# Performance work log

Measured on AMD Instinct MI355X. Metric: run time of the kernel, lower is better.

Reference implementation:

```python
import jax, jax.numpy as jnp
import numpy as np

FORGET_BIAS = 1.0  # TF BasicLSTMCell default


def setup_inputs() -> dict:
    key = jax.random.key(0)
    k1, k2, k3, k4 = jax.random.split(key, 4)
    B, T, E, H, V = 64, 128, 256, 1024, 32000
    x = jax.random.normal(k1, (B, T, E), dtype=jnp.float32)
    # fused LSTM kernel [(E+H), 4H], gate order i, j, f, o
    kernel = jax.random.normal(k2, (E + H, 4 * H), dtype=jnp.float32) * 0.05
    bias = jnp.zeros((4 * H,), dtype=jnp.float32)
    w_out = jax.random.normal(k3, (H, V), dtype=jnp.float32) * 0.01
    b_out = jax.random.normal(k4, (V,), dtype=jnp.float32)
    return {"x": x, "kernel": kernel, "bias": bias, "w_out": w_out, "b_out": b_out}


def _lstm_last_hidden(x, kernel, bias):
    B, T, E = x.shape
    H = kernel.shape[1] // 4
    c0 = jnp.zeros((B, H), dtype=x.dtype)
    h0 = jnp.zeros((B, H), dtype=x.dtype)

    def step(carry, x_t):
        c, h = carry
        gates = jnp.concatenate([x_t, h], axis=1) @ kernel + bias  # [B, 4H]
        i, j, f, o = jnp.split(gates, 4, axis=1)
        new_c = c * jax.nn.sigmoid(f + FORGET_BIAS) + jax.nn.sigmoid(i) * jnp.tanh(j)
        new_h = jnp.tanh(new_c) * jax.nn.sigmoid(o)
        return (new_c, new_h), None

    (c_T, h_T), _ = jax.lax.scan(step, (c0, h0), jnp.swapaxes(x, 0, 1))
    return h_T  # [B, H]


def reference(x, kernel, bias, w_out, b_out):
    h_last = _lstm_last_hidden(x, kernel, bias)
    return h_last @ w_out + b_out  # [B, V]
```

## Files before the change

### kernel.cpp

```cpp
#include <hip/hip_runtime.h>
#include <hip/hip_bf16.h>
#include <stdint.h>

#define B_ 64
#define T_ 128
#define E_ 256
#define H_ 1024
#define G_ 4096
#define V_ 32000
#define HS_ 65536

typedef __attribute__((ext_vector_type(8))) short short8;
typedef __attribute__((ext_vector_type(4))) float floatx4;

static __device__ __forceinline__ unsigned short f2bf(float f){
  union { float f; unsigned u; } v; v.f = f;
  unsigned r = v.u + 0x7FFFu + ((v.u >> 16) & 1u);
  return (unsigned short)(r >> 16);
}
static __device__ __forceinline__ float bf2f(unsigned short s){
  union { unsigned u; float f; } v; v.u = ((unsigned)s) << 16;
  return v.f;
}
static __device__ __forceinline__ float sigmoidf_(float x){
  return 1.0f / (1.0f + __expf(-x));
}
static __device__ __forceinline__ float tanhf_(float x){
  const float a = fabsf(x);
  const float t = 1.0f - 2.0f / (__expf(2.0f * a) + 1.0f);
  return __builtin_copysignf(t, x);
}

__global__ __launch_bounds__(256) void k_transpose(const float* __restrict__ kern,
    unsigned short* __restrict__ wx_t, unsigned short* __restrict__ wh_t){
  __shared__ float tile[32][36];
  const int k0 = blockIdx.x * 32, g0 = blockIdx.y * 32;
  const int r  = threadIdx.x >> 3;
  const int c4 = (threadIdx.x & 7) << 2;
  const float4 v = *reinterpret_cast<const float4*>(kern + (size_t)(k0 + r) * G_ + g0 + c4);
  tile[r][c4 + 0] = v.x; tile[r][c4 + 1] = v.y;
  tile[r][c4 + 2] = v.z; tile[r][c4 + 3] = v.w;
  __syncthreads();
  const unsigned short o0 = f2bf(tile[c4 + 0][r]);
  const unsigned short o1 = f2bf(tile[c4 + 1][r]);
  const unsigned short o2 = f2bf(tile[c4 + 2][r]);
  const unsigned short o3 = f2bf(tile[c4 + 3][r]);
  const ushort4 pk = make_ushort4(o0, o1, o2, o3);
  if (k0 < E_)
    *reinterpret_cast<ushort4*>(wx_t + (size_t)(g0 + r) * E_ + (k0 + c4)) = pk;
  else
    *reinterpret_cast<ushort4*>(wh_t + (size_t)(g0 + r) * H_ + (k0 - E_ + c4)) = pk;
}

__global__ __launch_bounds__(256) void k_xgates(const float* __restrict__ x,
    const unsigned short* __restrict__ wx_t, const float* __restrict__ bias,
    unsigned short* __restrict__ xgp){
  const int w = threadIdx.x >> 6, l = threadIdx.x & 63;
  const int quad = l >> 4, n = l & 15;
  const int Mbase = blockIdx.x * 64 + w * 16;
  const int Nbase = blockIdx.y * 256;
  const int r = Mbase + n;
  const int b = r & 63, t = r >> 6;
  const float* arow = x + ((size_t)b * T_ + t) * E_;
  floatx4 acc[16];
  #pragma unroll
  for (int i = 0; i < 16; ++i) acc[i] = (floatx4){0.f,0.f,0.f,0.f};
  #pragma unroll
  for (int kt = 0; kt < 8; ++kt){
    const int k0 = kt * 32 + quad * 8;
    const float4 f0 = *reinterpret_cast<const float4*>(arow + k0);
    const float4 f1 = *reinterpret_cast<const float4*>(arow + k0 + 4);
    short8 af;
    af[0] = (short)f2bf(f0.x); af[1] = (short)f2bf(f0.y);
    af[2] = (short)f2bf(f0.z); af[3] = (short)f2bf(f0.w);
    af[4] = (short)f2bf(f1.x); af[5] = (short)f2bf(f1.y);
    af[6] = (short)f2bf(f1.z); af[7] = (short)f2bf(f1.w);
    const unsigned short* bp = wx_t + (size_t)(Nbase + n) * E_ + k0;
    #pragma unroll
    for (int nt = 0; nt < 16; ++nt){
      const short8 bf = *reinterpret_cast<const short8*>(bp + (size_t)nt * 16 * E_);
      acc[nt] = __builtin_amdgcn_mfma_f32_16x16x32_bf16(af, bf, acc[nt], 0, 0, 0);
    }
  }
  const int t_out = blockIdx.x;
  const int gate = blockIdx.y >> 2;
  const int np = gate * 4 + (n & 3);
  #pragma unroll
  for (int nt = 0; nt < 16; ++nt){
    const int g = Nbase + nt * 16 + n;
    const float bi = bias[g];
    const int wgd = (blockIdx.y & 3) * 64 + nt * 4 + (n >> 2);
    ushort4 pk;
    pk.x = f2bf(acc[nt][0] + bi);
    pk.y = f2bf(acc[nt][1] + bi);
    pk.z = f2bf(acc[nt][2] + bi);
    pk.w = f2bf(acc[nt][3] + bi);
    *reinterpret_cast<ushort4*>(xgp +
        (((size_t)t_out * 256 + wgd) * 256 + w * 64 + quad * 16 + np) * 4) = pk;
  }
}

__global__ __launch_bounds__(256, 1) void k_lstm(const unsigned short* __restrict__ wh_t,
    const unsigned short* __restrict__ xgp, unsigned short* __restrict__ hb,
    float* __restrict__ hT, unsigned int* __restrict__ bar){
  const int tid = threadIdx.x;
  const int wg = blockIdx.x;
  const int hbase = wg * 4;
  const int w = tid >> 6, l = tid & 63, quad = l >> 4, n = l & 15;
  const int g_lane = (n >> 2) * H_ + hbase + (n & 3);
  const int rowb = w * 16 + quad * 4;
  const bool low8  = (n & 8) == 0;
  const bool first = (n & 4) == 0;

  short8 bfr[32];
  {
    const unsigned short* bp = wh_t + (size_t)g_lane * H_ + quad * 8;
    #pragma unroll
    for (int kt = 0; kt < 32; ++kt)
      bfr[kt] = *reinterpret_cast<const short8*>(bp + kt * 32);
  }
  #pragma unroll
  for (int kt = 0; kt < 32; ++kt)
    __asm__ volatile("" : "+a"(bfr[kt]));

  float creg[4] = {0.f, 0.f, 0.f, 0.f};
  ushort4 xgv = *reinterpret_cast<const ushort4*>(xgp + ((size_t)wg * 256 + tid) * 4);

  for (int t = 0; t < T_; ++t){
    const unsigned short* asrc = hb + (size_t)t * HS_ + (size_t)(w * 16 + n) * H_ + quad * 8;
    short8 afr[32];
    #pragma unroll
    for (int kt = 0; kt < 32; ++kt)
      afr[kt] = *reinterpret_cast<const short8*>(asrc + kt * 32);
    #pragma unroll
    for (int kt = 0; kt < 32; ++kt)
      __asm__ volatile("" : "+v"(afr[kt]));

    floatx4 a0 = {0.f,0.f,0.f,0.f}, a1 = {0.f,0.f,0.f,0.f};
    floatx4 a2 = {0.f,0.f,0.f,0.f}, a3 = {0.f,0.f,0.f,0.f};
    #pragma unroll
    for (int kt = 0; kt < 32; kt += 4){
      a0 = __builtin_amdgcn_mfma_f32_16x16x32_bf16(afr[kt + 0], bfr[kt + 0], a0, 0, 0, 0);
      a1 = __builtin_amdgcn_mfma_f32_16x16x32_bf16(afr[kt + 1], bfr[kt + 1], a1, 0, 0, 0);
      a2 = __builtin_amdgcn_mfma_f32_16x16x32_bf16(afr[kt + 2], bfr[kt + 2], a2, 0, 0, 0);
      a3 = __builtin_amdgcn_mfma_f32_16x16x32_bf16(afr[kt + 3], bfr[kt + 3], a3, 0, 0, 0);
    }
    floatx4 acc = (a0 + a1) + (a2 + a3);
    acc[0] += bf2f(xgv.x); acc[1] += bf2f(xgv.y);
    acc[2] += bf2f(xgv.z); acc[3] += bf2f(xgv.w);

    float r1o[4], q1[4], q2[4];
    #pragma unroll
    for (int reg = 0; reg < 4; ++reg){
      const float a_ = acc[reg];
      const float p_ = __shfl_xor(a_, 4);
      const float x1 = first ? a_ : p_;
      const float x2 = first ? p_ : a_;
      const float s1 = sigmoidf_(low8 ? x1 : (x1 + 1.0f));
      const float r1 = low8 ? s1 * tanhf_(x2) : s1;
      const float r2 = low8 ? 0.0f : sigmoidf_(x2);
      r1o[reg] = r1;
      q1[reg] = __shfl_xor(r1, 8);
      q2[reg] = __shfl_xor(r2, 8);
    }
    if (n < 4){
      unsigned short* hout = hb + (size_t)(t + 1) * HS_;
      #pragma unroll
      for (int reg = 0; reg < 4; ++reg){
        const float cn = creg[reg] * q1[reg] + r1o[reg];
        creg[reg] = cn;
        const float hv = tanhf_(cn) * q2[reg];
        __hip_atomic_store(&hout[(size_t)(rowb + reg) * H_ + hbase + n], f2bf(hv),
                           __ATOMIC_RELAXED, __HIP_MEMORY_SCOPE_AGENT);
        if (t == T_ - 1) hT[(size_t)(hbase + n) * B_ + rowb + reg] = hv;
      }
    }
    if (t < T_ - 1){
      const ushort4 xgv_n = *reinterpret_cast<const ushort4*>(
          xgp + (((size_t)(t + 1) * 256 + wg) * 256 + tid) * 4);
      __syncthreads();
      if (tid == 0){
        const unsigned step = (unsigned)(t + 1);
        __asm__ volatile("" ::: "memory");
        __hip_atomic_fetch_add(&bar[(wg & 15) * 32], 1u,
                               __ATOMIC_RELAXED, __HIP_MEMORY_SCOPE_AGENT);
        if (wg == 0){
          const unsigned tgt = step * 256u;
          unsigned s;
          do {
            s = 0;
            #pragma unroll
            for (int i = 0; i < 16; ++i)
              s += __hip_atomic_load(&bar[i * 32],
                                     __ATOMIC_RELAXED, __HIP_MEMORY_SCOPE_AGENT);
          } while (s < tgt);
          #pragma unroll
          for (int i = 0; i < 16; ++i)
            __hip_atomic_store(&bar[512 + i * 32], step,
                               __ATOMIC_RELAXED, __HIP_MEMORY_SCOPE_AGENT);
        } else {
          while (__hip_atomic_load(&bar[512 + (wg & 15) * 32],
                                   __ATOMIC_RELAXED, __HIP_MEMORY_SCOPE_AGENT) < step) {}
        }
        __asm__ volatile("" ::: "memory");
      }
      __syncthreads();
      xgv = xgv_n;
    }
  }
}

__global__ __launch_bounds__(256) void k_proj(const float* __restrict__ w_out,
    const float* __restrict__ hT, const float* __restrict__ b_out,
    float* __restrict__ out){
  __shared__ float wsh[32 * 68];
  __shared__ float hsh[32 * 68];
  const int tid = threadIdx.x;
  const int vbase = blockIdx.x * 64;
  const int vq = tid & 15, bg = tid >> 4;
  floatx4 acc[4] = {{0,0,0,0},{0,0,0,0},{0,0,0,0},{0,0,0,0}};
  for (int c = 0; c < 32; ++c){
    const int k0 = c * 32;
    __syncthreads();
    #pragma unroll
    for (int i = 0; i < 2; ++i){
      const int flat = tid + i * 256;
      const int row = flat >> 4, c4 = (flat & 15) << 2;
      *reinterpret_cast<float4*>(&wsh[row * 68 + c4]) =
        *reinterpret_cast<const float4*>(w_out + (size_t)(k0 + row) * V_ + vbase + c4);
      *reinterpret_cast<float4*>(&hsh[row * 68 + c4]) =
        *reinterpret_cast<const float4*>(hT + (size_t)(k0 + row) * B_ + c4);
    }
    __syncthreads();
    #pragma unroll 8
    for (int k = 0; k < 32; ++k){
      const floatx4 wv = *reinterpret_cast<const floatx4*>(&wsh[k * 68 + vq * 4]);
      #pragma unroll
      for (int j = 0; j < 4; ++j){
        acc[j] += hsh[k * 68 + bg * 4 + j] * wv;
      }
    }
  }
  const floatx4 bv = *reinterpret_cast<const floatx4*>(b_out + vbase + vq * 4);
  #pragma unroll
  for (int j = 0; j < 4; ++j){
    *reinterpret_cast<floatx4*>(out + (size_t)(bg * 4 + j) * V_ + vbase + vq * 4) = acc[j] + bv;
  }
}

extern "C" void kernel_launch(void* const* d_in, const int* in_sizes, int n_in,
                              void* d_out, int out_size, void* d_ws, size_t ws_size,
                              hipStream_t stream){
  (void)in_sizes; (void)n_in; (void)out_size; (void)ws_size;
  const float* x     = (const float*)d_in[0];
  const float* kern  = (const float*)d_in[1];
  const float* bias  = (const float*)d_in[2];
  const float* w_out = (const float*)d_in[3];
  const float* b_out = (const float*)d_in[4];
  float* out = (float*)d_out;
  char* ws = (char*)d_ws;

  const size_t BAR_OFF = 0;
  const size_t HB_OFF  = 4096;
  const size_t HT_OFF  = HB_OFF + (size_t)129 * 131072;
  const size_t WX_OFF  = HT_OFF + 262144;
  const size_t WH_OFF  = WX_OFF + 2097152;
  const size_t XG_OFF  = WH_OFF + 8388608;

  unsigned int*   bar  = (unsigned int*)(ws + BAR_OFF);
  unsigned short* hb   = (unsigned short*)(ws + HB_OFF);
  float*          hT   = (float*)(ws + HT_OFF);
  unsigned short* wx_t = (unsigned short*)(ws + WX_OFF);
  unsigned short* wh_t = (unsigned short*)(ws + WH_OFF);
  unsigned short* xgp  = (unsigned short*)(ws + XG_OFF);

  hipMemsetAsync(ws, 0, HB_OFF + 131072, stream);
  k_transpose<<<dim3(40, 128), 256, 0, stream>>>(kern, wx_t, wh_t);
  k_xgates<<<dim3(128, 16), 256, 0, stream>>>(x, wx_t, bias, xgp);
  k_lstm<<<dim3(256), 256, 0, stream>>>(wh_t, xgp, hb, hT, bar);
  k_proj<<<dim3(500), 256, 0, stream>>>(w_out, hT, b_out, out);
}
```

Baseline: 1.229 ms.

## Replace centralized grid barrier with split-half distributed counter waits

Replaces the master-block grid barrier (block 0 sums counters, then broadcasts a release flag) with a decentralized scheme. Each block increments a counter in one of two groups, chosen by which half of the hidden units it produces. Every thread then polls the group counters itself before loading the matching half of h. The first half of the K dimension can be loaded as soon as the first 128 producer blocks finish, so the broadcast hop is gone and loads overlap with the remaining producers. In exchange, all threads spin on global atomics with s_sleep, which adds memory traffic, and the trailing __syncthreads is removed.

```diff
diff --git a/kernel.cpp b/kernel.cpp
--- a/kernel.cpp
+++ b/kernel.cpp
@@ -111,6 +111,7 @@
   const int rowb = w * 16 + quad * 4;
   const bool low8  = (n & 8) == 0;
   const bool first = (n & 4) == 0;
+  const int grp_line = ((wg >> 7) * 16 + (wg & 15)) * 32;
 
   short8 bfr[32];
   {
@@ -129,11 +130,45 @@
   for (int t = 0; t < T_; ++t){
     const unsigned short* asrc = hb + (size_t)t * HS_ + (size_t)(w * 16 + n) * H_ + quad * 8;
     short8 afr[32];
-    #pragma unroll
-    for (int kt = 0; kt < 32; ++kt)
+
+    if (t){
+      const unsigned tgt = (unsigned)t * 128u;
+      unsigned s;
+      for (;;){
+        s = 0;
+        #pragma unroll
+        for (int i = 0; i < 16; ++i)
+          s += __hip_atomic_load(&bar[i * 32], __ATOMIC_RELAXED, __HIP_MEMORY_SCOPE_AGENT);
+        if (s >= tgt) break;
+        __builtin_amdgcn_s_sleep(1);
+      }
+      __asm__ volatile("" ::: "memory");
+    }
+    #pragma unroll
+    for (int kt = 0; kt < 16; ++kt)
       afr[kt] = *reinterpret_cast<const short8*>(asrc + kt * 32);
     #pragma unroll
-    for (int kt = 0; kt < 32; ++kt)
+    for (int kt = 0; kt < 16; ++kt)
+      __asm__ volatile("" : "+v"(afr[kt]));
+
+    if (t){
+      const unsigned tgt = (unsigned)t * 128u;
+      unsigned s;
+      for (;;){
+        s = 0;
+        #pragma unroll
+        for (int i = 0; i < 16; ++i)
+          s += __hip_atomic_load(&bar[(16 + i) * 32], __ATOMIC_RELAXED, __HIP_MEMORY_SCOPE_AGENT);
+        if (s >= tgt) break;
+        __builtin_amdgcn_s_sleep(1);
+      }
+      __asm__ volatile("" ::: "memory");
+    }
+    #pragma unroll
+    for (int kt = 16; kt < 32; ++kt)
+      afr[kt] = *reinterpret_cast<const short8*>(asrc + kt * 32);
+    #pragma unroll
+    for (int kt = 16; kt < 32; ++kt)
       __asm__ volatile("" : "+v"(afr[kt]));
 
     floatx4 a0 = {0.f,0.f,0.f,0.f}, a1 = {0.f,0.f,0.f,0.f};
@@ -180,31 +215,10 @@
           xgp + (((size_t)(t + 1) * 256 + wg) * 256 + tid) * 4);
       __syncthreads();
       if (tid == 0){
-        const unsigned step = (unsigned)(t + 1);
         __asm__ volatile("" ::: "memory");
-        __hip_atomic_fetch_add(&bar[(wg & 15) * 32], 1u,
+        __hip_atomic_fetch_add(&bar[grp_line], 1u,
                                __ATOMIC_RELAXED, __HIP_MEMORY_SCOPE_AGENT);
-        if (wg == 0){
-          const unsigned tgt = step * 256u;
-          unsigned s;
-          do {
-            s = 0;
-            #pragma unroll
-            for (int i = 0; i < 16; ++i)
-              s += __hip_atomic_load(&bar[i * 32],
-                                     __ATOMIC_RELAXED, __HIP_MEMORY_SCOPE_AGENT);
-          } while (s < tgt);
-          #pragma unroll
-          for (int i = 0; i < 16; ++i)
-            __hip_atomic_store(&bar[512 + i * 32], step,
-                               __ATOMIC_RELAXED, __HIP_MEMORY_SCOPE_AGENT);
-        } else {
-          while (__hip_atomic_load(&bar[512 + (wg & 15) * 32],
-                                   __ATOMIC_RELAXED, __HIP_MEMORY_SCOPE_AGENT) < step) {}
-        }
-        __asm__ volatile("" ::: "memory");
-      }
-      __syncthreads();
+      }
       xgv = xgv_n;
     }
   }
```

Measured after the change: 1.474 ms. 1.2x slower.

## Halve LSTM persistent blocks by assigning two hidden slices per workgroup

Applied to the files above, without the earlier changes.

Each persistent LSTM workgroup now owns two 4-column hidden slices instead of one, so the grid drops from 256 to 128 blocks and the grid barrier target is halved. The A fragments of h loaded from global memory are reused across both slices' MFMAs, which halves the total re-reading of h per step and the number of barrier participants. In exchange each block holds 64 B-fragments in AGPRs, runs twice the MFMA work per step, and uses only half the CUs.

```diff
diff --git a/kernel.cpp b/kernel.cpp
--- a/kernel.cpp
+++ b/kernel.cpp
@@ -105,26 +105,27 @@
     float* __restrict__ hT, unsigned int* __restrict__ bar){
   const int tid = threadIdx.x;
   const int wg = blockIdx.x;
-  const int hbase = wg * 4;
   const int w = tid >> 6, l = tid & 63, quad = l >> 4, n = l & 15;
-  const int g_lane = (n >> 2) * H_ + hbase + (n & 3);
   const int rowb = w * 16 + quad * 4;
   const bool low8  = (n & 8) == 0;
   const bool first = (n & 4) == 0;
 
-  short8 bfr[32];
-  {
+  short8 bfr[64];
+  #pragma unroll
+  for (int s = 0; s < 2; ++s){
+    const int g_lane = (n >> 2) * H_ + (2 * wg + s) * 4 + (n & 3);
     const unsigned short* bp = wh_t + (size_t)g_lane * H_ + quad * 8;
     #pragma unroll
     for (int kt = 0; kt < 32; ++kt)
-      bfr[kt] = *reinterpret_cast<const short8*>(bp + kt * 32);
-  }
-  #pragma unroll
-  for (int kt = 0; kt < 32; ++kt)
+      bfr[s * 32 + kt] = *reinterpret_cast<const short8*>(bp + kt * 32);
+  }
+  #pragma unroll
+  for (int kt = 0; kt < 64; ++kt)
     __asm__ volatile("" : "+a"(bfr[kt]));
 
-  float creg[4] = {0.f, 0.f, 0.f, 0.f};
-  ushort4 xgv = *reinterpret_cast<const ushort4*>(xgp + ((size_t)wg * 256 + tid) * 4);
+  float creg[2][4] = {{0.f,0.f,0.f,0.f},{0.f,0.f,0.f,0.f}};
+  ushort4 xgv0 = *reinterpret_cast<const ushort4*>(xgp + (((size_t)2 * wg + 0) * 256 + tid) * 4);
+  ushort4 xgv1 = *reinterpret_cast<const ushort4*>(xgp + (((size_t)2 * wg + 1) * 256 + tid) * 4);
 
   for (int t = 0; t < T_; ++t){
     const unsigned short* asrc = hb + (size_t)t * HS_ + (size_t)(w * 16 + n) * H_ + quad * 8;
@@ -136,48 +137,68 @@
     for (int kt = 0; kt < 32; ++kt)
       __asm__ volatile("" : "+v"(afr[kt]));
 
-    floatx4 a0 = {0.f,0.f,0.f,0.f}, a1 = {0.f,0.f,0.f,0.f};
-    floatx4 a2 = {0.f,0.f,0.f,0.f}, a3 = {0.f,0.f,0.f,0.f};
+    floatx4 p0 = {0.f,0.f,0.f,0.f}, p1 = {0.f,0.f,0.f,0.f};
+    floatx4 p2 = {0.f,0.f,0.f,0.f}, p3 = {0.f,0.f,0.f,0.f};
+    floatx4 q0 = {0.f,0.f,0.f,0.f}, q1_ = {0.f,0.f,0.f,0.f};
+    floatx4 q2_ = {0.f,0.f,0.f,0.f}, q3 = {0.f,0.f,0.f,0.f};
     #pragma unroll
     for (int kt = 0; kt < 32; kt += 4){
-      a0 = __builtin_amdgcn_mfma_f32_16x16x32_bf16(afr[kt + 0], bfr[kt + 0], a0, 0, 0, 0);
-      a1 = __builtin_amdgcn_mfma_f32_16x16x32_bf16(afr[kt + 1], bfr[kt + 1], a1, 0, 0, 0);
-      a2 = __builtin_amdgcn_mfma_f32_16x16x32_bf16(afr[kt + 2], bfr[kt + 2], a2, 0, 0, 0);
-      a3 = __builtin_amdgcn_mfma_f32_16x16x32_bf16(afr[kt + 3], bfr[kt + 3], a3, 0, 0, 0);
-    }
-    floatx4 acc = (a0 + a1) + (a2 + a3);
-    acc[0] += bf2f(xgv.x); acc[1] += bf2f(xgv.y);
-    acc[2] += bf2f(xgv.z); acc[3] += bf2f(xgv.w);
-
-    float r1o[4], q1[4], q2[4];
-    #pragma unroll
-    for (int reg = 0; reg < 4; ++reg){
-      const float a_ = acc[reg];
-      const float p_ = __shfl_xor(a_, 4);
-      const float x1 = first ? a_ : p_;
-      const float x2 = first ? p_ : a_;
-      const float s1 = sigmoidf_(low8 ? x1 : (x1 + 1.0f));
-      const float r1 = low8 ? s1 * tanhf_(x2) : s1;
-      const float r2 = low8 ? 0.0f : sigmoidf_(x2);
-      r1o[reg] = r1;
-      q1[reg] = __shfl_xor(r1, 8);
-      q2[reg] = __shfl_xor(r2, 8);
-    }
-    if (n < 4){
-      unsigned short* hout = hb + (size_t)(t + 1) * HS_;
+      p0  = __builtin_amdgcn_mfma_f32_16x16x32_bf16(afr[kt + 0], bfr[kt + 0],      p0, 0, 0, 0);
+      q0  = __builtin_amdgcn_mfma_f32_16x16x32_bf16(afr[kt + 0], bfr[32 + kt + 0], q0, 0, 0, 0);
+      p1  = __builtin_amdgcn_mfma_f32_16x16x32_bf16(afr[kt + 1], bfr[kt + 1],      p1, 0, 0, 0);
+      q1_ = __builtin_amdgcn_mfma_f32_16x16x32_bf16(afr[kt + 1], bfr[32 + kt + 1], q1_, 0, 0, 0);
+      p2  = __builtin_amdgcn_mfma_f32_16x16x32_bf16(afr[kt + 2], bfr[kt + 2],      p2, 0, 0, 0);
+      q2_ = __builtin_amdgcn_mfma_f32_16x16x32_bf16(afr[kt + 2], bfr[32 + kt + 2], q2_, 0, 0, 0);
+      p3  = __builtin_amdgcn_mfma_f32_16x16x32_bf16(afr[kt + 3], bfr[kt + 3],      p3, 0, 0, 0);
+      q3  = __builtin_amdgcn_mfma_f32_16x16x32_bf16(afr[kt + 3], bfr[32 + kt + 3], q3, 0, 0, 0);
+    }
+    floatx4 acc[2];
+    acc[0] = (p0 + p1) + (p2 + p3);
+    acc[1] = (q0 + q1_) + (q2_ + q3);
+    acc[0][0] += bf2f(xgv0.x); acc[0][1] += bf2f(xgv0.y);
+    acc[0][2] += bf2f(xgv0.z); acc[0][3] += bf2f(xgv0.w);
+    acc[1][0] += bf2f(xgv1.x); acc[1][1] += bf2f(xgv1.y);
+    acc[1][2] += bf2f(xgv1.z); acc[1][3] += bf2f(xgv1.w);
+
+    ushort4 xgv0n, xgv1n;
+    if (t < T_ - 1){
+      xgv0n = *reinterpret_cast<const ushort4*>(
+          xgp + (((size_t)(t + 1) * 256 + 2 * wg + 0) * 256 + tid) * 4);
+      xgv1n = *reinterpret_cast<const ushort4*>(
+          xgp + (((size_t)(t + 1) * 256 + 2 * wg + 1) * 256 + tid) * 4);
+    }
+
+    #pragma unroll
+    for (int s = 0; s < 2; ++s){
+      float r1o[4], g1[4], g2[4];
       #pragma unroll
       for (int reg = 0; reg < 4; ++reg){
-        const float cn = creg[reg] * q1[reg] + r1o[reg];
-        creg[reg] = cn;
-        const float hv = tanhf_(cn) * q2[reg];
-        __hip_atomic_store(&hout[(size_t)(rowb + reg) * H_ + hbase + n], f2bf(hv),
-                           __ATOMIC_RELAXED, __HIP_MEMORY_SCOPE_AGENT);
-        if (t == T_ - 1) hT[(size_t)(hbase + n) * B_ + rowb + reg] = hv;
+        const float a_ = acc[s][reg];
+        const float p_ = __shfl_xor(a_, 4);
+        const float x1 = first ? a_ : p_;
+        const float x2 = first ? p_ : a_;
+        const float s1 = sigmoidf_(low8 ? x1 : (x1 + 1.0f));
+        const float r1 = low8 ? s1 * tanhf_(x2) : s1;
+        const float r2 = low8 ? 0.0f : sigmoidf_(x2);
+        r1o[reg] = r1;
+        g1[reg] = __shfl_xor(r1, 8);
+        g2[reg] = __shfl_xor(r2, 8);
       }
+      if (n < 4){
+        const int hb_s = (2 * wg + s) * 4;
+        unsigned short* hout = hb + (size_t)(t + 1) * HS_;
+        #pragma unroll
+        for (int reg = 0; reg < 4; ++reg){
+          const float cn = creg[s][reg] * g1[reg] + r1o[reg];
+          creg[s][reg] = cn;
+          const float hv = tanhf_(cn) * g2[reg];
+          __hip_atomic_store(&hout[(size_t)(rowb + reg) * H_ + hb_s + n], f2bf(hv),
+                             __ATOMIC_RELAXED, __HIP_MEMORY_SCOPE_AGENT);
+          if (t == T_ - 1) hT[(size_t)(hb_s + n) * B_ + rowb + reg] = hv;
+        }
+      }
     }
     if (t < T_ - 1){
-      const ushort4 xgv_n = *reinterpret_cast<const ushort4*>(
-          xgp + (((size_t)(t + 1) * 256 + wg) * 256 + tid) * 4);
       __syncthreads();
       if (tid == 0){
         const unsigned step = (unsigned)(t + 1);
@@ -185,7 +206,7 @@
         __hip_atomic_fetch_add(&bar[(wg & 15) * 32], 1u,
                                __ATOMIC_RELAXED, __HIP_MEMORY_SCOPE_AGENT);
         if (wg == 0){
-          const unsigned tgt = step * 256u;
+          const unsigned tgt = step * 128u;
           unsigned s;
           do {
             s = 0;
@@ -205,7 +226,7 @@
         __asm__ volatile("" ::: "memory");
       }
       __syncthreads();
-      xgv = xgv_n;
+      xgv0 = xgv0n; xgv1 = xgv1n;
     }
   }
 }
@@ -277,6 +298,6 @@
   hipMemsetAsync(ws, 0, HB_OFF + 131072, stream);
   k_transpose<<<dim3(40, 128), 256, 0, stream>>>(kern, wx_t, wh_t);
   k_xgates<<<dim3(128, 16), 256, 0, stream>>>(x, wx_t, bias, xgp);
-  k_lstm<<<dim3(256), 256, 0, stream>>>(wh_t, xgp, hb, hT, bar);
+  k_lstm<<<dim3(128), 256, 0, stream>>>(wh_t, xgp, hb, hT, bar);
   k_proj<<<dim3(500), 256, 0, stream>>>(w_out, hT, b_out, out);
 }
```

Result: slower. 1.362 ms (+10.8%).

## Spread grid barrier counters over 64 slots and reduce them with wave shuffles

Applied to the files above, without the earlier changes.

The grid-wide step barrier now spreads arrival atomics across 64 padded counters instead of 16, which cuts contention on each counter. The master workgroup's first wavefront loads all 64 in parallel and sums them with cross-lane shuffles instead of looping serially over loads. The next step's xgates prefetch is also moved ahead of the MFMA loop so its latency overlaps with compute. The workspace offset grows to fit the larger barrier area, and the master block still adds a spin round-trip on the critical path of every step.

```diff
diff --git a/kernel.cpp b/kernel.cpp
--- a/kernel.cpp
+++ b/kernel.cpp
@@ -12,6 +12,7 @@
 
 typedef __attribute__((ext_vector_type(8))) short short8;
 typedef __attribute__((ext_vector_type(4))) float floatx4;
+typedef __attribute__((ext_vector_type(4))) unsigned short ushortx4;
 
 static __device__ __forceinline__ unsigned short f2bf(float f){
   union { float f; unsigned u; } v; v.f = f;
@@ -124,7 +125,7 @@
     __asm__ volatile("" : "+a"(bfr[kt]));
 
   float creg[4] = {0.f, 0.f, 0.f, 0.f};
-  ushort4 xgv = *reinterpret_cast<const ushort4*>(xgp + ((size_t)wg * 256 + tid) * 4);
+  ushortx4 xgv = *reinterpret_cast<const ushortx4*>(xgp + ((size_t)wg * 256 + tid) * 4);
 
   for (int t = 0; t < T_; ++t){
     const unsigned short* asrc = hb + (size_t)t * HS_ + (size_t)(w * 16 + n) * H_ + quad * 8;
@@ -135,6 +136,13 @@
     #pragma unroll
     for (int kt = 0; kt < 32; ++kt)
       __asm__ volatile("" : "+v"(afr[kt]));
+
+    ushortx4 xgv_n = xgv;
+    if (t < T_ - 1){
+      xgv_n = *reinterpret_cast<const ushortx4*>(
+          xgp + (((size_t)(t + 1) * 256 + wg) * 256 + tid) * 4);
+      __asm__ volatile("" : "+v"(xgv_n));
+    }
 
     floatx4 a0 = {0.f,0.f,0.f,0.f}, a1 = {0.f,0.f,0.f,0.f};
     floatx4 a2 = {0.f,0.f,0.f,0.f}, a3 = {0.f,0.f,0.f,0.f};
@@ -146,8 +154,8 @@
       a3 = __builtin_amdgcn_mfma_f32_16x16x32_bf16(afr[kt + 3], bfr[kt + 3], a3, 0, 0, 0);
     }
     floatx4 acc = (a0 + a1) + (a2 + a3);
-    acc[0] += bf2f(xgv.x); acc[1] += bf2f(xgv.y);
-    acc[2] += bf2f(xgv.z); acc[3] += bf2f(xgv.w);
+    acc[0] += bf2f(xgv[0]); acc[1] += bf2f(xgv[1]);
+    acc[2] += bf2f(xgv[2]); acc[3] += bf2f(xgv[3]);
 
     float r1o[4], q1[4], q2[4];
     #pragma unroll
@@ -176,32 +184,31 @@
       }
     }
     if (t < T_ - 1){
-      const ushort4 xgv_n = *reinterpret_cast<const ushort4*>(
-          xgp + (((size_t)(t + 1) * 256 + wg) * 256 + tid) * 4);
       __syncthreads();
+      const unsigned step = (unsigned)(t + 1);
       if (tid == 0){
-        const unsigned step = (unsigned)(t + 1);
         __asm__ volatile("" ::: "memory");
-        __hip_atomic_fetch_add(&bar[(wg & 15) * 32], 1u,
+        __hip_atomic_fetch_add(&bar[(wg & 63) * 32], 1u,
                                __ATOMIC_RELAXED, __HIP_MEMORY_SCOPE_AGENT);
-        if (wg == 0){
+      }
+      if (wg == 0){
+        if (tid < 64){
           const unsigned tgt = step * 256u;
-          unsigned s;
-          do {
-            s = 0;
-            #pragma unroll
-            for (int i = 0; i < 16; ++i)
-              s += __hip_atomic_load(&bar[i * 32],
-                                     __ATOMIC_RELAXED, __HIP_MEMORY_SCOPE_AGENT);
-          } while (s < tgt);
-          #pragma unroll
-          for (int i = 0; i < 16; ++i)
-            __hip_atomic_store(&bar[512 + i * 32], step,
+          for (;;){
+            unsigned s = __hip_atomic_load(&bar[tid * 32],
+                                           __ATOMIC_RELAXED, __HIP_MEMORY_SCOPE_AGENT);
+            s += __shfl_xor(s, 1);  s += __shfl_xor(s, 2);
+            s += __shfl_xor(s, 4);  s += __shfl_xor(s, 8);
+            s += __shfl_xor(s, 16); s += __shfl_xor(s, 32);
+            if (s >= tgt) break;
+          }
+          if (tid < 16)
+            __hip_atomic_store(&bar[2048 + tid * 32], step,
                                __ATOMIC_RELAXED, __HIP_MEMORY_SCOPE_AGENT);
-        } else {
-          while (__hip_atomic_load(&bar[512 + (wg & 15) * 32],
-                                   __ATOMIC_RELAXED, __HIP_MEMORY_SCOPE_AGENT) < step) {}
         }
+      } else if (tid == 0){
+        while (__hip_atomic_load(&bar[2048 + (wg & 15) * 32],
+                                 __ATOMIC_RELAXED, __HIP_MEMORY_SCOPE_AGENT) < step) {}
         __asm__ volatile("" ::: "memory");
       }
       __syncthreads();
@@ -261,7 +268,7 @@
   char* ws = (char*)d_ws;
 
   const size_t BAR_OFF = 0;
-  const size_t HB_OFF  = 4096;
+  const size_t HB_OFF  = 16384;
   const size_t HT_OFF  = HB_OFF + (size_t)129 * 131072;
   const size_t WX_OFF  = HT_OFF + 262144;
   const size_t WH_OFF  = WX_OFF + 2097152;
```

New measurement: 1.269 ms. +3.3%, slower.
